# Performance work log

Hardware: AMD Instinct MI355X
Metric: run time of the kernel (lower is better)

The kernel has to match this reference:

```python
import jax, jax.numpy as jnp
import numpy as np

N_NODES = 50000
N_EDGES = 800000
IN_DIM = 128
OUT_DIM = 16
N_HEADS = 4
NEG_SLOPE = 0.01  # jax.nn.leaky_relu default, matches original


def setup_inputs() -> dict:
    key = jax.random.key(0)
    k = jax.random.split(key, 8)
    nodes = jax.random.normal(k[0], (N_NODES, IN_DIM), dtype=jnp.float32)
    edges = jax.random.uniform(k[1], (N_NODES, 1), dtype=jnp.float32)  # node-indexed edge attr (edges[senders] in source)
    senders = jax.random.randint(k[2], (N_EDGES,), 0, N_NODES, dtype=jnp.int32)
    receivers = jax.random.randint(k[3], (N_EDGES,), 0, N_NODES, dtype=jnp.int32)
    W = jax.random.normal(k[4], (N_HEADS * OUT_DIM, IN_DIM), dtype=jnp.float32) / np.sqrt(IN_DIM)
    b = jnp.zeros((N_HEADS * OUT_DIM,), dtype=jnp.float32)
    attn_W = jax.random.normal(k[5], (N_HEADS, 2 * OUT_DIM + 1), dtype=jnp.float32) / np.sqrt(2 * OUT_DIM + 1)
    attn_b = jnp.zeros((N_HEADS,), dtype=jnp.float32)
    return dict(nodes=nodes, edges=edges, senders=senders, receivers=receivers,
                W=W, b=b, attn_W=attn_W, attn_b=attn_b)


def _segment_softmax(logits, seg, num_segments):
    # logits: [E, H, 1]; softmax over edges sharing the same receiver
    m = jax.ops.segment_max(logits, seg, num_segments=num_segments)
    e = jnp.exp(logits - m[seg])
    s = jax.ops.segment_sum(e, seg, num_segments=num_segments)
    return e / s[seg]


def reference(nodes, edges, senders, receivers, W, b, attn_W, attn_b):
    n = nodes.shape[0]
    h = (nodes @ W.T + b).reshape(n, N_HEADS, OUT_DIM)       # [N, H, D]
    sent = h[senders]                                        # [E, H, D]
    recv = h[receivers]                                      # [E, H, D]
    sent_e = jnp.tile(edges[senders], (1, N_HEADS))[..., None]  # [E, H, 1]
    feat = jnp.concatenate([sent, recv, sent_e], axis=-1)    # [E, H, 2D+1]
    logits = (jnp.einsum('ehd,hd->eh', feat, attn_W) + attn_b)[..., None]  # [E, H, 1]
    logits = jax.nn.leaky_relu(logits, NEG_SLOPE)
    logits = logits * jnp.sum(sent_e)                        # scalar scaling as in source
    att = _segment_softmax(logits, receivers, n)             # [E, H, 1]
    msg = sent * att                                         # [E, H, D]
    out = jax.ops.segment_sum(msg, receivers, num_segments=n)  # [N, H, D]
    out = jax.nn.leaky_relu(out, NEG_SLOPE)                  # last=False branch
    return out.reshape(n, N_HEADS * OUT_DIM)
```

## Files before the change

### kernel.cpp

```cpp
#include <hip/hip_runtime.h>
#include <math.h>

#define N_NODES 50000
#define N_EDGES 800000
#define IN_DIM 128
#define OUT_DIM 16
#define N_HEADS 4
#define HID 64
#define AW_COLS 33
#define GN 32
#define GW 8
#define GEMM_BLK ((N_NODES + GN - 1) / GN)
#define HE 16
#define HBLK ((N_EDGES + 256 * HE - 1) / (256 * HE))
#define MAXDEG 64

__global__ __launch_bounds__(256) void gemm_hist(
    const float* __restrict__ nodes, const float* __restrict__ W,
    const float* __restrict__ b, const float* __restrict__ attn_W,
    const float* __restrict__ attn_b, const float* __restrict__ edges,
    float* __restrict__ h, double* __restrict__ z_src, double* __restrict__ z_dst,
    const int* __restrict__ senders, const int* __restrict__ receivers,
    int* __restrict__ counts, int* __restrict__ srt_padded,
    double* __restrict__ Ssum) {
    __shared__ float sW[HID * IN_DIM];
    __shared__ float sN[GN * IN_DIM];
    int t = threadIdx.x;

    if (blockIdx.x < HBLK) {
        double* red = (double*)sN;
        int base = blockIdx.x * 256 * HE + t;
        double sp = 0.0;
        #pragma unroll
        for (int j = 0; j < HE; ++j) {
            int e = base + j * 256;
            if (e < N_EDGES) {
                int r = receivers[e];
                int rank = atomicAdd(&counts[r], 1);
                if (rank < MAXDEG)
                    srt_padded[r * MAXDEG + rank] = senders[e];
                sp += (double)edges[senders[e]];
            }
        }
        red[t] = sp;
        __syncthreads();
        for (int off = 128; off > 0; off >>= 1) {
            if (t < off) red[t] += red[t + off];
            __syncthreads();
        }
        if (t == 0) atomicAdd(Ssum, red[0]);
    } else {
        for (int i4 = t; i4 < HID * IN_DIM / 4; i4 += 256) {
            int o = i4 >> 5, kq = i4 & 31;
            float4 v = ((const float4*)W)[i4];
            *(float4*)&sW[o * IN_DIM + (((kq + o) & 31) << 2)] = v;
        }
        int node0 = (blockIdx.x - HBLK) * GN;
        for (int i4 = t; i4 < GN * IN_DIM / 4; i4 += 256) {
            int ln = i4 >> 5;
            int n = node0 + ln;
            float4 v = (n < N_NODES) ? ((const float4*)nodes)[(long long)n * (IN_DIM / 4) + (i4 & 31)]
                                     : make_float4(0.f, 0.f, 0.f, 0.f);
            *(float4*)&sN[i4 << 2] = v;
        }
        __syncthreads();
        int w = t >> 6, o = t & 63;
        double acc[GW];
        #pragma unroll
        for (int j = 0; j < GW; ++j) acc[j] = (double)b[o];
        const float* wrow = &sW[o * IN_DIM];
        const float* nbase = &sN[(w * GW) * IN_DIM];
        for (int kq = 0; kq < 32; ++kq) {
            float4 wv = *(const float4*)&wrow[((kq + o) & 31) << 2];
            double wx = (double)wv.x, wy = (double)wv.y;
            double wz = (double)wv.z, ww = (double)wv.w;
            #pragma unroll
            for (int j = 0; j < GW; ++j) {
                float4 nv = *(const float4*)&nbase[j * IN_DIM + (kq << 2)];
                acc[j] += wx * (double)nv.x;
                acc[j] += wy * (double)nv.y;
                acc[j] += wz * (double)nv.z;
                acc[j] += ww * (double)nv.w;
            }
        }
        int hd = o >> 4, d = o & 15;
        double aw0 = (double)attn_W[hd * AW_COLS + d];
        double aw1 = (double)attn_W[hd * AW_COLS + OUT_DIM + d];
        double wE  = (double)attn_W[hd * AW_COLS + 2 * OUT_DIM];
        double bbh = (double)attn_b[hd];
        #pragma unroll
        for (int j = 0; j < GW; ++j) {
            int n = node0 + w * GW + j;
            if (n >= N_NODES) break;
            float hf = (float)acc[j];
            h[(long long)n * HID + o] = hf;
            double c0 = (double)hf * aw0;
            double c1 = (double)hf * aw1;
            #pragma unroll
            for (int k = 1; k <= 8; k <<= 1) {
                c0 += __shfl_xor(c0, k, 64);
                c1 += __shfl_xor(c1, k, 64);
            }
            if (d == 0) {
                double se = (double)edges[n];
                z_src[n * N_HEADS + hd] = c0 + se * wE;
                z_dst[n * N_HEADS + hd] = c1 + bbh;
            }
        }
    }
}

__global__ __launch_bounds__(256) void node_fused(
    const float* __restrict__ h, const double* __restrict__ z_src,
    const double* __restrict__ z_dst,
    const int* __restrict__ srt_padded, const int* __restrict__ counts,
    const double* __restrict__ Ssum, float* __restrict__ out) {
    int node = blockIdx.x * 4 + (threadIdx.x >> 6);
    int lane = threadIdx.x & 63;
    if (node >= N_NODES) return;
    int hd = lane >> 4, q = lane & 15;
    int deg = counts[node];
    if (deg > MAXDEG) deg = MAXDEG;
    long long obase = (long long)node * HID + lane;
    if (deg <= 0) { out[obase] = 0.f; return; }
    const int* srow = srt_padded + node * MAXDEG;

    double S = 4.0 * Ssum[0];
    double zdn = z_dst[node * N_HEADS + hd];
    float m_run;
    float den = 0.f, acc = 0.f;

    int s[4];
    float y[4], ev[4];
    #pragma unroll
    for (int j = 0; j < 4; ++j) {
        int ei = q + 16 * j;
        y[j] = -INFINITY;
        s[j] = 0;
        if (ei < deg) {
            s[j] = srow[ei];
            double yy = z_src[(long long)s[j] * N_HEADS + hd] + zdn;
            yy = yy > 0.0 ? yy : 0.01 * yy;
            y[j] = (float)yy;
        }
    }
    float mv = fmaxf(fmaxf(y[0], y[1]), fmaxf(y[2], y[3]));
    #pragma unroll
    for (int k = 1; k <= 8; k <<= 1)
        mv = fmaxf(mv, __shfl_xor(mv, k, 64));
    m_run = mv;
    float dsum = 0.f;
    #pragma unroll
    for (int j = 0; j < 4; ++j) {
        ev[j] = (y[j] == -INFINITY) ? 0.f
              : __expf((float)(S * ((double)y[j] - (double)m_run)));
        dsum += ev[j];
    }
    #pragma unroll
    for (int k = 1; k <= 8; k <<= 1)
        dsum += __shfl_xor(dsum, k, 64);
    den += dsum;
    #pragma unroll
    for (int j = 0; j < 4; ++j) {
        unsigned long long mk = __ballot(ev[j] != 0.f);
        unsigned um = (unsigned)((mk | (mk >> 16) | (mk >> 32) | (mk >> 48)) & 0xFFFFull);
        while (um) {
            int qq = __builtin_ctz(um);
            um &= um - 1;
            int src = (lane & 48) | qq;
            float evv = __shfl(ev[j], src, 64);
            int sj = __shfl(s[j], src, 64);
            if (evv != 0.f)
                acc = fmaf(evv, h[(long long)sj * HID + lane], acc);
        }
    }
    float r = (den > 0.f) ? acc / den : 0.f;
    out[obase] = r > 0.f ? r : 0.01f * r;
}

static inline char* ws_take(char*& p, size_t bytes) {
    char* cur = p;
    p += (bytes + 255) & ~(size_t)255;
    return cur;
}

extern "C" void kernel_launch(void* const* d_in, const int* in_sizes, int n_in,
                              void* d_out, int out_size, void* d_ws, size_t ws_size,
                              hipStream_t stream) {
    const float* nodes     = (const float*)d_in[0];
    const float* edges     = (const float*)d_in[1];
    const int*   senders   = (const int*)d_in[2];
    const int*   receivers = (const int*)d_in[3];
    const float* W         = (const float*)d_in[4];
    const float* b         = (const float*)d_in[5];
    const float* attn_W    = (const float*)d_in[6];
    const float* attn_b    = (const float*)d_in[7];
    float* out = (float*)d_out;

    char* p = (char*)d_ws;
    float*  h          = (float*)ws_take(p, sizeof(float) * N_NODES * HID);
    double* z_src      = (double*)ws_take(p, sizeof(double) * N_NODES * N_HEADS);
    double* z_dst      = (double*)ws_take(p, sizeof(double) * N_NODES * N_HEADS);
    int*    counts     = (int*)ws_take(p, sizeof(int) * N_NODES);
    char*   zpad       = ws_take(p, 256);
    double* Ssum       = (double*)zpad;
    int*    srt_padded = (int*)ws_take(p, sizeof(int) * (size_t)N_NODES * MAXDEG);

    hipMemsetAsync(counts, 0, ((sizeof(int) * N_NODES + 255) & ~(size_t)255) + 256, stream);

    gemm_hist<<<HBLK + GEMM_BLK, 256, 0, stream>>>(
        nodes, W, b, attn_W, attn_b, edges, h, z_src, z_dst,
        senders, receivers, counts, srt_padded, Ssum);
    node_fused<<<(N_NODES + 3) / 4, 256, 0, stream>>>(
        h, z_src, z_dst, srt_padded, counts, Ssum, out);
}
```

Before: 167.9 us.

## Compute two output columns per thread in GEMM, raise node tile to 56

Register tiling in the fp64 GEMM changes so each thread computes two output features (o and o+32) over 7 nodes, instead of one feature over 8 nodes. Each shared-memory node load now feeds twice as many FMAs, and the block tile grows from 32 to 56 nodes, so fewer GEMM blocks are launched. The cost is more registers per thread (14 double accumulators plus 8 weights) and a larger sN shared buffer, which may reduce occupancy.

```diff
diff --git a/kernel.cpp b/kernel.cpp
--- a/kernel.cpp
+++ b/kernel.cpp
@@ -8,8 +8,7 @@
 #define N_HEADS 4
 #define HID 64
 #define AW_COLS 33
-#define GN 32
-#define GW 8
+#define GN 56
 #define GEMM_BLK ((N_NODES + GN - 1) / GN)
 #define HE 16
 #define HBLK ((N_EDGES + 256 * HE - 1) / (256 * HE))
@@ -64,47 +63,68 @@
             *(float4*)&sN[i4 << 2] = v;
         }
         __syncthreads();
-        int w = t >> 6, o = t & 63;
-        double acc[GW];
+        int w = t >> 6, l = t & 63;
+        int half = l >> 5;
+        int o2 = l & 31;
+        int nwbase = w * 14 + half * 7;
+        double acc0[7], acc1[7];
+        double b0 = (double)b[o2], b1 = (double)b[o2 + 32];
         #pragma unroll
-        for (int j = 0; j < GW; ++j) acc[j] = (double)b[o];
-        const float* wrow = &sW[o * IN_DIM];
-        const float* nbase = &sN[(w * GW) * IN_DIM];
+        for (int j = 0; j < 7; ++j) { acc0[j] = b0; acc1[j] = b1; }
+        const float* wrow0 = &sW[o2 * IN_DIM];
+        const float* wrow1 = &sW[(o2 + 32) * IN_DIM];
+        const float* nbase = &sN[nwbase * IN_DIM];
         for (int kq = 0; kq < 32; ++kq) {
-            float4 wv = *(const float4*)&wrow[((kq + o) & 31) << 2];
-            double wx = (double)wv.x, wy = (double)wv.y;
-            double wz = (double)wv.z, ww = (double)wv.w;
+            int rot = ((kq + o2) & 31) << 2;
+            float4 wv0 = *(const float4*)&wrow0[rot];
+            float4 wv1 = *(const float4*)&wrow1[rot];
+            double w0x = (double)wv0.x, w0y = (double)wv0.y, w0z = (double)wv0.z, w0w = (double)wv0.w;
+            double w1x = (double)wv1.x, w1y = (double)wv1.y, w1z = (double)wv1.z, w1w = (double)wv1.w;
             #pragma unroll
-            for (int j = 0; j < GW; ++j) {
+            for (int j = 0; j < 7; ++j) {
                 float4 nv = *(const float4*)&nbase[j * IN_DIM + (kq << 2)];
-                acc[j] += wx * (double)nv.x;
-                acc[j] += wy * (double)nv.y;
-                acc[j] += wz * (double)nv.z;
-                acc[j] += ww * (double)nv.w;
-            }
-        }
-        int hd = o >> 4, d = o & 15;
-        double aw0 = (double)attn_W[hd * AW_COLS + d];
-        double aw1 = (double)attn_W[hd * AW_COLS + OUT_DIM + d];
-        double wE  = (double)attn_W[hd * AW_COLS + 2 * OUT_DIM];
-        double bbh = (double)attn_b[hd];
+                double nx = (double)nv.x, ny = (double)nv.y;
+                double nz = (double)nv.z, nw = (double)nv.w;
+                acc0[j] += w0x * nx; acc0[j] += w0y * ny;
+                acc0[j] += w0z * nz; acc0[j] += w0w * nw;
+                acc1[j] += w1x * nx; acc1[j] += w1y * ny;
+                acc1[j] += w1z * nz; acc1[j] += w1w * nw;
+            }
+        }
+        int hd0 = o2 >> 4, d = o2 & 15;
+        int hd1 = hd0 + 2;
+        double aw00 = (double)attn_W[hd0 * AW_COLS + d];
+        double aw01 = (double)attn_W[hd0 * AW_COLS + OUT_DIM + d];
+        double aw10 = (double)attn_W[hd1 * AW_COLS + d];
+        double aw11 = (double)attn_W[hd1 * AW_COLS + OUT_DIM + d];
+        double wE0 = (double)attn_W[hd0 * AW_COLS + 2 * OUT_DIM];
+        double wE1 = (double)attn_W[hd1 * AW_COLS + 2 * OUT_DIM];
+        double bb0 = (double)attn_b[hd0], bb1 = (double)attn_b[hd1];
         #pragma unroll
-        for (int j = 0; j < GW; ++j) {
-            int n = node0 + w * GW + j;
-            if (n >= N_NODES) break;
-            float hf = (float)acc[j];
-            h[(long long)n * HID + o] = hf;
-            double c0 = (double)hf * aw0;
-            double c1 = (double)hf * aw1;
+        for (int j = 0; j < 7; ++j) {
+            int n = node0 + nwbase + j;
+            if (n >= N_NODES) continue;
+            float hf0 = (float)acc0[j];
+            float hf1 = (float)acc1[j];
+            h[(long long)n * HID + o2] = hf0;
+            h[(long long)n * HID + o2 + 32] = hf1;
+            double c00 = (double)hf0 * aw00;
+            double c01 = (double)hf0 * aw01;
+            double c10 = (double)hf1 * aw10;
+            double c11 = (double)hf1 * aw11;
             #pragma unroll
             for (int k = 1; k <= 8; k <<= 1) {
-                c0 += __shfl_xor(c0, k, 64);
-                c1 += __shfl_xor(c1, k, 64);
+                c00 += __shfl_xor(c00, k, 64);
+                c01 += __shfl_xor(c01, k, 64);
+                c10 += __shfl_xor(c10, k, 64);
+                c11 += __shfl_xor(c11, k, 64);
             }
             if (d == 0) {
                 double se = (double)edges[n];
-                z_src[n * N_HEADS + hd] = c0 + se * wE;
-                z_dst[n * N_HEADS + hd] = c1 + bbh;
+                z_src[n * N_HEADS + hd0] = c00 + se * wE0;
+                z_dst[n * N_HEADS + hd0] = c01 + bb0;
+                z_src[n * N_HEADS + hd1] = c10 + se * wE1;
+                z_dst[n * N_HEADS + hd1] = c11 + bb1;
             }
         }
     }
@@ -127,7 +147,6 @@
 
     double S = 4.0 * Ssum[0];
     double zdn = z_dst[node * N_HEADS + hd];
-    float m_run;
     float den = 0.f, acc = 0.f;
 
     int s[4];
@@ -148,7 +167,7 @@
     #pragma unroll
     for (int k = 1; k <= 8; k <<= 1)
         mv = fmaxf(mv, __shfl_xor(mv, k, 64));
-    m_run = mv;
+    float m_run = mv;
     float dsum = 0.f;
     #pragma unroll
     for (int j = 0; j < 4; ++j) {
```

Result: slower. 175.1 us (+4.3%).
